# Kernel optimization log

Measured on AMD Instinct MI355X. Metric: run time of the kernel, lower is better.

The kernel has to match this reference:

```python
import jax, jax.numpy as jnp
import numpy as np

NEG_SLOPE = 0.2  # PyG GATConv default negative_slope


def gat_conv(x, src, dst, W, a_src, a_dst, b, n_nodes, concat):
    # x: [N, F_in]; W: [F_in, H*C]; a_src/a_dst: [H, C]; b: [H*C] or [C]
    H, C = a_src.shape
    h = (x @ W).reshape(n_nodes, H, C)                      # [N, H, C]
    al_src = jnp.sum(h * a_src[None], axis=-1)              # [N, H]
    al_dst = jnp.sum(h * a_dst[None], axis=-1)              # [N, H]
    e = jax.nn.leaky_relu(al_src[src] + al_dst[dst], NEG_SLOPE)  # [E, H]
    # segment softmax over incoming edges of each destination node
    m = jax.ops.segment_max(e, dst, num_segments=n_nodes)  # [N, H]
    ex = jnp.exp(e - m[dst])                                # [E, H]
    s = jax.ops.segment_sum(ex, dst, num_segments=n_nodes)  # [N, H]
    alpha = ex / s[dst]                                     # [E, H]
    msg = h[src] * alpha[:, :, None]                        # [E, H, C]
    out = jax.ops.segment_sum(msg, dst, num_segments=n_nodes)  # [N, H, C]
    if concat:
        out = out.reshape(n_nodes, H * C)
    else:
        out = out.mean(axis=1)
    return out + b


def setup_inputs() -> dict:
    key = jax.random.key(0)
    ks = jax.random.split(key, 10)
    N, E = 100000, 800000
    F_in, C1, H, C2 = 128, 32, 8, 16
    x = jax.random.normal(ks[0], (N, F_in), dtype=jnp.float32)
    edge_index = jax.random.randint(ks[1], (2, E), 0, N, dtype=jnp.int64)
    s = 0.05
    return {
        "x": x,
        "edge_index": edge_index,
        "W1": jax.random.normal(ks[2], (F_in, H * C1), dtype=jnp.float32) * s,
        "att_src1": jax.random.normal(ks[3], (H, C1), dtype=jnp.float32) * s,
        "att_dst1": jax.random.normal(ks[4], (H, C1), dtype=jnp.float32) * s,
        "b1": jnp.zeros((H * C1,), dtype=jnp.float32),
        "W2": jax.random.normal(ks[5], (H * C1, H * C2), dtype=jnp.float32) * s,
        "att_src2": jax.random.normal(ks[6], (H, C2), dtype=jnp.float32) * s,
        "att_dst2": jax.random.normal(ks[7], (H, C2), dtype=jnp.float32) * s,
        "b2": jnp.zeros((C2,), dtype=jnp.float32),
    }


def reference(x, edge_index, W1, att_src1, att_dst1, b1, W2, att_src2, att_dst2, b2):
    n = x.shape[0]
    # PyG GATConv default add_self_loops=True (same augmented edge set for both layers)
    loops = jnp.arange(n, dtype=edge_index.dtype)
    src = jnp.concatenate([edge_index[0], loops])
    dst = jnp.concatenate([edge_index[1], loops])
    # dropout_p = 0.0 -> dropout is identity (eval-mode math)
    h = gat_conv(x, src, dst, W1, att_src1, att_dst1, b1, n, concat=True)
    h = jax.nn.elu(h)
    out = gat_conv(h, src, dst, W2, att_src2, att_dst2, b2, n, concat=False)
    return jax.nn.log_softmax(out, axis=-1)
```

## Files before the change

kernel.cpp:

```cpp
#include <hip/hip_runtime.h>
#include <cstdint>
#include <cstddef>


typedef short bf16x8 __attribute__((ext_vector_type(8)));
typedef unsigned short u16x8 __attribute__((ext_vector_type(8)));
typedef float f32x4 __attribute__((ext_vector_type(4)));

__device__ inline unsigned short f2bf(float f) {
  unsigned u = __float_as_uint(f);
  unsigned r = (u + 0x7FFFu + ((u >> 16) & 1u)) >> 16;
  return (unsigned short)r;
}
__device__ inline float bf2f(unsigned short s) {
  return __uint_as_float((unsigned)s << 16);
}

__device__ inline unsigned char fp8enc(float x) {
  unsigned u = __float_as_uint(x);
  unsigned s = u >> 31;
  float ax = fminf(fabsf(x), 448.f);
  unsigned em;
  if (ax >= 0.015625f) {
    unsigned b = __float_as_uint(ax);
    unsigned b2 = b + 0x7FFFFu + ((b >> 20) & 1u);
    em = (b2 >> 20) - 960u;
    if (em > 126u) em = 126u;
  } else {
    em = (unsigned)__float2int_rn(ax * 512.f);
  }
  return (unsigned char)((s << 7) | em);
}
__device__ inline float fp8dec_sw(unsigned b8) {
  unsigned s = b8 >> 7, em = b8 & 0x7Fu;
  float fn = __uint_as_float((s << 31) | ((em + 960u) << 20));
  float fd = (float)em * 0.001953125f;
  fd = s ? -fd : fd;
  return em >= 8u ? fn : fd;
}
__device__ inline void fp8dec4(unsigned w, float* out) {
#if __has_builtin(__builtin_amdgcn_cvt_f32_fp8)
  out[0] = __builtin_amdgcn_cvt_f32_fp8(w, 0);
  out[1] = __builtin_amdgcn_cvt_f32_fp8(w, 1);
  out[2] = __builtin_amdgcn_cvt_f32_fp8(w, 2);
  out[3] = __builtin_amdgcn_cvt_f32_fp8(w, 3);
#else
  out[0] = fp8dec_sw(w & 0xFFu);
  out[1] = fp8dec_sw((w >> 8) & 0xFFu);
  out[2] = fp8dec_sw((w >> 16) & 0xFFu);
  out[3] = fp8dec_sw((w >> 24) & 0xFFu);
#endif
}


__global__ __launch_bounds__(256) void detect_kernel(const int* __restrict__ words,
                                                     int E, int* __restrict__ flag) {
  int t = threadIdx.x;
  int n = E < 1024 ? E : 1024;
  int cnt = 0;
  for (int i = t; i < n; i += 256) cnt += (words[2 * i + 1] != 0) ? 1 : 0;
  for (int m = 1; m < 64; m <<= 1) cnt += __shfl_xor(cnt, m);
  if ((t & 63) == 0 && cnt) atomicAdd(flag, cnt);
}

__global__ __launch_bounds__(256) void extract_kernel(const void* __restrict__ ei,
                                                      int E, int N,
                                                      const int* __restrict__ flag,
                                                      int* __restrict__ src,
                                                      int* __restrict__ dst,
                                                      int* __restrict__ deg) {
  int e = blockIdx.x * 256 + threadIdx.x;
  int ET = E + N;
  if (e >= ET) return;
  int s, d;
  if (e < E) {
    if (flag[0] == 0) {
      const long long* p = (const long long*)ei;
      s = (int)p[e];
      d = (int)p[(size_t)E + e];
    } else {
      const int* p = (const int*)ei;
      s = p[e];
      d = p[E + e];
    }
  } else {
    s = d = e - E;
  }
  src[e] = s;
  dst[e] = d;
  atomicAdd(&deg[d], 1);
}

__global__ __launch_bounds__(256) void scan_a(const int* __restrict__ deg,
                                              int* __restrict__ off,
                                              int* __restrict__ bsum, int N) {
  __shared__ int sh[256];
  int b = blockIdx.x, t = threadIdx.x;
  int base = b * 2048 + t * 8;
  int p[8];
  int run = 0;
#pragma unroll
  for (int j = 0; j < 8; ++j) {
    int v = (base + j < N) ? deg[base + j] : 0;
    run += v;
    p[j] = run;
  }
  sh[t] = run;
  __syncthreads();
  for (int d = 1; d < 256; d <<= 1) {
    int x = (t >= d) ? sh[t - d] : 0;
    __syncthreads();
    if (t >= d) sh[t] += x;
    __syncthreads();
  }
  int excl = sh[t] - run;
#pragma unroll
  for (int j = 0; j < 8; ++j)
    if (base + j < N) off[base + j + 1] = excl + p[j];
  if (t == 255) bsum[b] = sh[255];
}

__global__ void scan_b(int* __restrict__ bsum, int nb) {
  int t = threadIdx.x;
  int orig = (t < nb) ? bsum[t] : 0;
  int v = orig;
  for (int d = 1; d < 64; d <<= 1) {
    int u = __shfl_up(v, d);
    if (t >= d) v += u;
  }
  if (t < nb) bsum[t] = v - orig;
}

__global__ __launch_bounds__(256) void scan_c(int* __restrict__ off,
                                              const int* __restrict__ bsum, int N) {
  int i = blockIdx.x * 256 + threadIdx.x;
  if (i == 0) off[0] = 0;
  if (i >= 1 && i <= N) off[i] += bsum[(i - 1) / 2048];
}

__global__ __launch_bounds__(256) void fill_kernel(const int* __restrict__ src,
                                                   const int* __restrict__ dst,
                                                   const int* __restrict__ off,
                                                   int* __restrict__ deg,
                                                   int* __restrict__ csr, int ET) {
  int e = blockIdx.x * 256 + threadIdx.x;
  if (e >= ET) return;
  int d = dst[e];
  int p = atomicSub(&deg[d], 1) - 1;
  csr[off[d] + p] = src[e];
}

__global__ __launch_bounds__(256) void pack_kernel(const float* __restrict__ W,
                                                   short* __restrict__ Wp,
                                                   int NOUT, int total) {
  int NT = NOUT >> 4;
  for (int idx = blockIdx.x * 256 + threadIdx.x; idx < total;
       idx += gridDim.x * 256) {
    int j = idx & 7;
    int lane = (idx >> 3) & 63;
    int st = idx >> 9;
    int s = st / NT, t = st - s * NT;
    int k = s * 32 + (lane >> 4) * 8 + j;
    int n = t * 16 + (lane & 15);
    Wp[idx] = (short)f2bf(W[(size_t)k * NOUT + n]);
  }
}

template <int K, int NOUT, bool AF32, bool OUT_FP8>
__global__ __launch_bounds__(256) void mfma_gemm(const void* __restrict__ Av,
                                                 const short* __restrict__ Bp,
                                                 short* __restrict__ Cb,
                                                 unsigned char* __restrict__ Cq,
                                                 const float* __restrict__ as,
                                                 const float* __restrict__ ad,
                                                 float* __restrict__ alsO,
                                                 float* __restrict__ aldO, int M) {
  constexpr int KS = K / 32;
  constexpr int NT = NOUT / 16;
  constexpr int RST = NOUT + 8;
  constexpr int QST = NOUT + 16;
  constexpr int C = NOUT / 8;
  __shared__ __align__(16) short lds[64 * RST];
  __shared__ __align__(16) unsigned char ldsq[OUT_FP8 ? 64 * QST : 16];
  const int tid = threadIdx.x;
  const int wave = tid >> 6, lane = tid & 63;
  const int lo = lane & 15, hi = lane >> 4;
  const int rowA = blockIdx.x * 64 + wave * 16 + lo;
  const bool inb = rowA < M;

  f32x4 acc[NT];
#pragma unroll
  for (int t = 0; t < NT; ++t) acc[t] = (f32x4){0.f, 0.f, 0.f, 0.f};

#pragma unroll
  for (int s = 0; s < KS; ++s) {
    bf16x8 af;
    if constexpr (AF32) {
      const float* Ap = (const float*)Av;
      float v[8];
      if (inb) {
        const float4 x0 = *(const float4*)&Ap[(size_t)rowA * K + s * 32 + hi * 8];
        const float4 x1 = *(const float4*)&Ap[(size_t)rowA * K + s * 32 + hi * 8 + 4];
        v[0] = x0.x; v[1] = x0.y; v[2] = x0.z; v[3] = x0.w;
        v[4] = x1.x; v[5] = x1.y; v[6] = x1.z; v[7] = x1.w;
      } else {
#pragma unroll
        for (int j = 0; j < 8; ++j) v[j] = 0.f;
      }
#pragma unroll
      for (int j = 0; j < 8; ++j) af[j] = (short)f2bf(v[j]);
    } else {
      const short* Ab = (const short*)Av;
      if (inb) {
        af = *(const bf16x8*)&Ab[(size_t)rowA * K + s * 32 + hi * 8];
      } else {
#pragma unroll
        for (int j = 0; j < 8; ++j) af[j] = 0;
      }
    }
#pragma unroll
    for (int t = 0; t < NT; ++t) {
      bf16x8 bf = *(const bf16x8*)&Bp[((size_t)(s * NT + t) * 64 + lane) * 8];
      acc[t] = __builtin_amdgcn_mfma_f32_16x16x32_bf16(af, bf, acc[t], 0, 0, 0);
    }
  }

#pragma unroll
  for (int t = 0; t < NT; ++t)
#pragma unroll
    for (int r = 0; r < 4; ++r) {
      int row = wave * 16 + hi * 4 + r;
      lds[row * RST + t * 16 + lo] = (short)f2bf(acc[t][r]);
      if constexpr (OUT_FP8)
        ldsq[row * QST + t * 16 + lo] = fp8enc(acc[t][r]);
    }
  __syncthreads();

  if constexpr (OUT_FP8) {
#pragma unroll
    for (int i = 0; i < (64 * NOUT / 16) / 256; ++i) {
      int v = i * 256 + tid;
      int r = v >> 4;
      int c = v & 15;
      int grow = blockIdx.x * 64 + r;
      if (grow < M)
        *(float4*)&Cq[(size_t)grow * NOUT + c * 16] =
            *(const float4*)&ldsq[r * QST + c * 16];
    }
  } else {
    constexpr int VECS = 64 * NOUT / 8;
#pragma unroll
    for (int i = 0; i < VECS / 256; ++i) {
      int v = i * 256 + tid;
      int r = v / (NOUT / 8);
      int c = v % (NOUT / 8);
      int grow = blockIdx.x * 64 + r;
      if (grow < M)
        *(float4*)&Cb[(size_t)grow * NOUT + c * 8] =
            *(const float4*)&lds[r * RST + c * 8];
    }
  }

  constexpr int SEGS = NOUT / 64;
  if (tid < 64 * SEGS) {
    int r = tid / SEGS, seg = tid % SEGS;
    int grow = blockIdx.x * 64 + r;
    float ps[8], pd[8];
#pragma unroll
    for (int k = 0; k < 8; ++k) { ps[k] = 0.f; pd[k] = 0.f; }
#pragma unroll
    for (int k = 0; k < 8; ++k) {
      int b = seg + SEGS * k;
      u16x8 u = *(const u16x8*)&lds[r * RST + b * 8];
#pragma unroll
      for (int j = 0; j < 8; ++j) {
        float hv = bf2f(u[j]);
        ps[k] = fmaf(hv, as[k * C + seg * 8 + j], ps[k]);
        pd[k] = fmaf(hv, ad[k * C + seg * 8 + j], pd[k]);
      }
    }
#pragma unroll
    for (int d = 1; d < SEGS; d <<= 1)
#pragma unroll
      for (int k = 0; k < 8; ++k) {
        ps[k] += __shfl_xor(ps[k], d);
        pd[k] += __shfl_xor(pd[k], d);
      }
    if (seg == 0 && grow < M) {
      *(float4*)&alsO[(size_t)grow * 8] = make_float4(ps[0], ps[1], ps[2], ps[3]);
      *(float4*)&alsO[(size_t)grow * 8 + 4] = make_float4(ps[4], ps[5], ps[6], ps[7]);
      *(float4*)&aldO[(size_t)grow * 8] = make_float4(pd[0], pd[1], pd[2], pd[3]);
      *(float4*)&aldO[(size_t)grow * 8 + 4] = make_float4(pd[4], pd[5], pd[6], pd[7]);
    }
  }
}

__global__ __launch_bounds__(256) void agg1_kernel(const unsigned char* __restrict__ hq,
                                                   const float* __restrict__ als,
                                                   const float* __restrict__ ald,
                                                   const int* __restrict__ off,
                                                   const int* __restrict__ csr,
                                                   const float* __restrict__ bias,
                                                   short* __restrict__ outb, int N) {
  int wid = blockIdx.x * 4 + (threadIdx.x >> 6);
  if (wid >= N) return;
  int lane = threadIdx.x & 63;
  int rs = off[wid], re = off[wid + 1];
  int es = lane >> 5;
  int gl = lane & 31;
  int head = gl >> 2;
  float aldv = ald[wid * 8 + head];

  float acc[8];
#pragma unroll
  for (int j = 0; j < 8; ++j) acc[j] = 0.f;
  float ws = 0.f;

  int i = rs + es;
  for (; i + 2 < re; i += 4) {
    int s0 = csr[i], s1 = csr[i + 2];
    float e0 = als[s0 * 8 + head] + aldv;
    float e1 = als[s1 * 8 + head] + aldv;
    uint2 u0 = *(const uint2*)&hq[(size_t)s0 * 256 + gl * 8];
    uint2 u1 = *(const uint2*)&hq[(size_t)s1 * 256 + gl * 8];
    e0 = e0 > 0.f ? e0 : 0.2f * e0;
    e1 = e1 > 0.f ? e1 : 0.2f * e1;
    float w0 = __expf(e0), w1 = __expf(e1);
    ws += w0 + w1;
    float d0a[4], d0b[4], d1a[4], d1b[4];
    fp8dec4(u0.x, d0a); fp8dec4(u0.y, d0b);
    fp8dec4(u1.x, d1a); fp8dec4(u1.y, d1b);
#pragma unroll
    for (int j = 0; j < 4; ++j) {
      acc[j] = fmaf(w0, d0a[j], acc[j]);
      acc[j + 4] = fmaf(w0, d0b[j], acc[j + 4]);
      acc[j] = fmaf(w1, d1a[j], acc[j]);
      acc[j + 4] = fmaf(w1, d1b[j], acc[j + 4]);
    }
  }
  if (i < re) {
    int s0 = csr[i];
    float e0 = als[s0 * 8 + head] + aldv;
    uint2 u0 = *(const uint2*)&hq[(size_t)s0 * 256 + gl * 8];
    e0 = e0 > 0.f ? e0 : 0.2f * e0;
    float w0 = __expf(e0);
    ws += w0;
    float d0a[4], d0b[4];
    fp8dec4(u0.x, d0a); fp8dec4(u0.y, d0b);
#pragma unroll
    for (int j = 0; j < 4; ++j) {
      acc[j] = fmaf(w0, d0a[j], acc[j]);
      acc[j + 4] = fmaf(w0, d0b[j], acc[j + 4]);
    }
  }

  ws += __shfl_xor(ws, 32);
#pragma unroll
  for (int j = 0; j < 8; ++j) acc[j] += __shfl_xor(acc[j], 32);
  float inv = 1.f / ws;

  if (lane < 32) {
    u16x8 o;
#pragma unroll
    for (int j = 0; j < 8; ++j) {
      float v = acc[j] * inv + bias[gl * 8 + j];
      o[j] = f2bf(v > 0.f ? v : expm1f(v));
    }
    *(u16x8*)&outb[(size_t)wid * 256 + gl * 8] = o;
  }
}

__global__ __launch_bounds__(256) void agg2_kernel(const short* __restrict__ hb,
                                                   const float* __restrict__ als,
                                                   const float* __restrict__ ald,
                                                   const int* __restrict__ off,
                                                   const int* __restrict__ csr,
                                                   const float* __restrict__ bias,
                                                   float* __restrict__ out, int N) {
  constexpr int LPG = 16;
  constexpr int NS = 4;
  int wid = blockIdx.x * 4 + (threadIdx.x >> 6);
  if (wid >= N) return;
  int lane = threadIdx.x & 63;
  int rs = off[wid], re = off[wid + 1];
  int es = lane / LPG;
  int gl = lane & (LPG - 1);
  int head = gl >> 1;
  float aldv = ald[wid * 8 + head];

  float acc[8];
#pragma unroll
  for (int j = 0; j < 8; ++j) acc[j] = 0.f;
  float ws = 0.f;

  int i = rs + es;
  for (; i + NS < re; i += 2 * NS) {
    int s0 = csr[i], s1 = csr[i + NS];
    float e0 = als[s0 * 8 + head] + aldv;
    float e1 = als[s1 * 8 + head] + aldv;
    u16x8 u0 = *(const u16x8*)&hb[(size_t)s0 * 128 + gl * 8];
    u16x8 u1 = *(const u16x8*)&hb[(size_t)s1 * 128 + gl * 8];
    e0 = e0 > 0.f ? e0 : 0.2f * e0;
    e1 = e1 > 0.f ? e1 : 0.2f * e1;
    float w0 = __expf(e0), w1 = __expf(e1);
    ws += w0 + w1;
#pragma unroll
    for (int j = 0; j < 8; ++j)
      acc[j] = fmaf(w1, bf2f(u1[j]), fmaf(w0, bf2f(u0[j]), acc[j]));
  }
  if (i < re) {
    int s0 = csr[i];
    float e0 = als[s0 * 8 + head] + aldv;
    u16x8 u0 = *(const u16x8*)&hb[(size_t)s0 * 128 + gl * 8];
    e0 = e0 > 0.f ? e0 : 0.2f * e0;
    float w0 = __expf(e0);
    ws += w0;
#pragma unroll
    for (int j = 0; j < 8; ++j) acc[j] = fmaf(w0, bf2f(u0[j]), acc[j]);
  }

#pragma unroll
  for (int d = LPG; d < 64; d <<= 1) {
    ws += __shfl_xor(ws, d);
#pragma unroll
    for (int j = 0; j < 8; ++j) acc[j] += __shfl_xor(acc[j], d);
  }
  float inv = 1.f / ws;

#pragma unroll
  for (int j = 0; j < 8; ++j) acc[j] *= inv;
#pragma unroll
  for (int d = 2; d <= 8; d <<= 1)
#pragma unroll
    for (int j = 0; j < 8; ++j) acc[j] += __shfl_xor(acc[j], d);
  int p = gl & 1;
  float v[8];
#pragma unroll
  for (int j = 0; j < 8; ++j) v[j] = acc[j] * 0.125f + bias[p * 8 + j];
  float m = v[0];
#pragma unroll
  for (int j = 1; j < 8; ++j) m = fmaxf(m, v[j]);
  m = fmaxf(m, __shfl_xor(m, 1));
  float se = 0.f;
#pragma unroll
  for (int j = 0; j < 8; ++j) se += __expf(v[j] - m);
  se += __shfl_xor(se, 1);
  float lse = m + logf(se);
  if (lane < 2) {
    *(float4*)&out[(size_t)wid * 16 + p * 8] =
        make_float4(v[0] - lse, v[1] - lse, v[2] - lse, v[3] - lse);
    *(float4*)&out[(size_t)wid * 16 + p * 8 + 4] =
        make_float4(v[4] - lse, v[5] - lse, v[6] - lse, v[7] - lse);
  }
}


extern "C" void kernel_launch(void* const* d_in, const int* in_sizes, int n_in,
                              void* d_out, int out_size, void* d_ws, size_t ws_size,
                              hipStream_t stream) {
  const float* x = (const float*)d_in[0];
  const void* ei = d_in[1];
  const float* W1 = (const float*)d_in[2];
  const float* as1 = (const float*)d_in[3];
  const float* ad1 = (const float*)d_in[4];
  const float* b1 = (const float*)d_in[5];
  const float* W2 = (const float*)d_in[6];
  const float* as2 = (const float*)d_in[7];
  const float* ad2 = (const float*)d_in[8];
  const float* b2 = (const float*)d_in[9];
  float* out = (float*)d_out;

  const int N = out_size / 16;
  const int E = in_sizes[1] / 2;
  const int ET = E + N;

  char* p = (char*)d_ws;
  auto alloc = [&](size_t bytes) {
    char* r = p;
    p += (bytes + 255) & ~(size_t)255;
    return (void*)r;
  };
  unsigned char* h1q = (unsigned char*)alloc((size_t)N * 256);
  short* hactb = (short*)alloc((size_t)N * 256 * 2);
  short* h2b = (short*)alloc((size_t)N * 128 * 2);
  float* als = (float*)alloc((size_t)N * 8 * 4);
  float* ald = (float*)alloc((size_t)N * 8 * 4);
  int* src32 = (int*)alloc((size_t)ET * 4);
  int* dst32 = (int*)alloc((size_t)ET * 4);
  int* csr = (int*)alloc((size_t)ET * 4);
  int* deg = (int*)alloc((size_t)N * 4);
  int* off = (int*)alloc((size_t)(N + 1) * 4);
  int* bsum = (int*)alloc(256 * 4);
  int* flag = (int*)alloc(256);
  short* W1p = (short*)alloc(128 * 256 * 2);
  short* W2p = (short*)alloc(256 * 128 * 2);

  hipMemsetAsync(deg, 0, (size_t)N * 4, stream);
  hipMemsetAsync(flag, 0, 4, stream);

  detect_kernel<<<1, 256, 0, stream>>>((const int*)ei, E, flag);
  int gridET = (ET + 255) / 256;
  extract_kernel<<<gridET, 256, 0, stream>>>(ei, E, N, flag, src32, dst32, deg);
  int nscan = (N + 2047) / 2048;
  scan_a<<<nscan, 256, 0, stream>>>(deg, off, bsum, N);
  scan_b<<<1, 64, 0, stream>>>(bsum, nscan);
  scan_c<<<(N + 256) / 256, 256, 0, stream>>>(off, bsum, N);
  fill_kernel<<<gridET, 256, 0, stream>>>(src32, dst32, off, deg, csr, ET);

  pack_kernel<<<128, 256, 0, stream>>>(W1, W1p, 256, 128 * 256);
  pack_kernel<<<128, 256, 0, stream>>>(W2, W2p, 128, 256 * 128);

  int gemmGrid = (N + 63) / 64;
  int nodeGrid = (N + 3) / 4;

  mfma_gemm<128, 256, true, true><<<gemmGrid, 256, 0, stream>>>(
      x, W1p, nullptr, h1q, as1, ad1, als, ald, N);
  agg1_kernel<<<nodeGrid, 256, 0, stream>>>(h1q, als, ald, off, csr, b1, hactb, N);
  mfma_gemm<256, 128, false, false><<<gemmGrid, 256, 0, stream>>>(
      hactb, W2p, h2b, nullptr, as2, ad2, als, ald, N);
  agg2_kernel<<<nodeGrid, 256, 0, stream>>>(h2b, als, ald, off, csr, b2, out, N);
}
```

Baseline: 338.5 us.

## Store layer-2 features in fp8 and widen per-lane gathers in aggregation

Layer 2's GEMM now emits fp8 features, reusing the layer-1 fp8 buffer, instead of bf16, so agg2 gathers half the bytes per neighbor. agg1 is restructured so 16 lanes each load 16 bytes per edge and four edge streams run per wave, instead of 32 lanes loading 8 bytes. The two memsets are merged into one by moving the flag allocation next to deg. The aim is to cut the gather traffic that dominates aggregation, at the cost of extra fp8 quantization error in layer 2 and more registers in agg1.

```diff
diff --git a/kernel.cpp b/kernel.cpp
--- a/kernel.cpp
+++ b/kernel.cpp
@@ -237,11 +237,12 @@
   __syncthreads();
 
   if constexpr (OUT_FP8) {
-#pragma unroll
-    for (int i = 0; i < (64 * NOUT / 16) / 256; ++i) {
+    constexpr int CPR = NOUT / 16;
+#pragma unroll
+    for (int i = 0; i < (64 * CPR) / 256; ++i) {
       int v = i * 256 + tid;
-      int r = v >> 4;
-      int c = v & 15;
+      int r = v / CPR;
+      int c = v % CPR;
       int grow = blockIdx.x * 64 + r;
       if (grow < M)
         *(float4*)&Cq[(size_t)grow * NOUT + c * 16] =
@@ -306,85 +307,85 @@
   if (wid >= N) return;
   int lane = threadIdx.x & 63;
   int rs = off[wid], re = off[wid + 1];
-  int es = lane >> 5;
-  int gl = lane & 31;
-  int head = gl >> 2;
+  int es = lane >> 4;
+  int gl = lane & 15;
+  int head = gl >> 1;
   float aldv = ald[wid * 8 + head];
 
-  float acc[8];
-#pragma unroll
-  for (int j = 0; j < 8; ++j) acc[j] = 0.f;
+  float acc[16];
+#pragma unroll
+  for (int j = 0; j < 16; ++j) acc[j] = 0.f;
   float ws = 0.f;
 
   int i = rs + es;
-  for (; i + 2 < re; i += 4) {
-    int s0 = csr[i], s1 = csr[i + 2];
+  for (; i + 4 < re; i += 8) {
+    int s0 = csr[i], s1 = csr[i + 4];
     float e0 = als[s0 * 8 + head] + aldv;
     float e1 = als[s1 * 8 + head] + aldv;
-    uint2 u0 = *(const uint2*)&hq[(size_t)s0 * 256 + gl * 8];
-    uint2 u1 = *(const uint2*)&hq[(size_t)s1 * 256 + gl * 8];
+    uint4 u0 = *(const uint4*)&hq[(size_t)s0 * 256 + gl * 16];
+    uint4 u1 = *(const uint4*)&hq[(size_t)s1 * 256 + gl * 16];
     e0 = e0 > 0.f ? e0 : 0.2f * e0;
     e1 = e1 > 0.f ? e1 : 0.2f * e1;
     float w0 = __expf(e0), w1 = __expf(e1);
     ws += w0 + w1;
-    float d0a[4], d0b[4], d1a[4], d1b[4];
-    fp8dec4(u0.x, d0a); fp8dec4(u0.y, d0b);
-    fp8dec4(u1.x, d1a); fp8dec4(u1.y, d1b);
-#pragma unroll
-    for (int j = 0; j < 4; ++j) {
-      acc[j] = fmaf(w0, d0a[j], acc[j]);
-      acc[j + 4] = fmaf(w0, d0b[j], acc[j + 4]);
-      acc[j] = fmaf(w1, d1a[j], acc[j]);
-      acc[j + 4] = fmaf(w1, d1b[j], acc[j + 4]);
-    }
+    float d0[16], d1[16];
+    fp8dec4(u0.x, d0); fp8dec4(u0.y, d0 + 4);
+    fp8dec4(u0.z, d0 + 8); fp8dec4(u0.w, d0 + 12);
+    fp8dec4(u1.x, d1); fp8dec4(u1.y, d1 + 4);
+    fp8dec4(u1.z, d1 + 8); fp8dec4(u1.w, d1 + 12);
+#pragma unroll
+    for (int j = 0; j < 16; ++j)
+      acc[j] = fmaf(w1, d1[j], fmaf(w0, d0[j], acc[j]));
   }
   if (i < re) {
     int s0 = csr[i];
     float e0 = als[s0 * 8 + head] + aldv;
-    uint2 u0 = *(const uint2*)&hq[(size_t)s0 * 256 + gl * 8];
+    uint4 u0 = *(const uint4*)&hq[(size_t)s0 * 256 + gl * 16];
     e0 = e0 > 0.f ? e0 : 0.2f * e0;
     float w0 = __expf(e0);
     ws += w0;
-    float d0a[4], d0b[4];
-    fp8dec4(u0.x, d0a); fp8dec4(u0.y, d0b);
-#pragma unroll
-    for (int j = 0; j < 4; ++j) {
-      acc[j] = fmaf(w0, d0a[j], acc[j]);
-      acc[j + 4] = fmaf(w0, d0b[j], acc[j + 4]);
-    }
-  }
-
-  ws += __shfl_xor(ws, 32);
-#pragma unroll
-  for (int j = 0; j < 8; ++j) acc[j] += __shfl_xor(acc[j], 32);
+    float d0[16];
+    fp8dec4(u0.x, d0); fp8dec4(u0.y, d0 + 4);
+    fp8dec4(u0.z, d0 + 8); fp8dec4(u0.w, d0 + 12);
+#pragma unroll
+    for (int j = 0; j < 16; ++j) acc[j] = fmaf(w0, d0[j], acc[j]);
+  }
+
+#pragma unroll
+  for (int d = 16; d < 64; d <<= 1) {
+    ws += __shfl_xor(ws, d);
+#pragma unroll
+    for (int j = 0; j < 16; ++j) acc[j] += __shfl_xor(acc[j], d);
+  }
   float inv = 1.f / ws;
 
-  if (lane < 32) {
-    u16x8 o;
+  if (lane < 16) {
+    u16x8 o0, o1;
 #pragma unroll
     for (int j = 0; j < 8; ++j) {
-      float v = acc[j] * inv + bias[gl * 8 + j];
-      o[j] = f2bf(v > 0.f ? v : expm1f(v));
-    }
-    *(u16x8*)&outb[(size_t)wid * 256 + gl * 8] = o;
-  }
-}
-
-__global__ __launch_bounds__(256) void agg2_kernel(const short* __restrict__ hb,
+      float v0 = acc[j] * inv + bias[gl * 16 + j];
+      float v1 = acc[j + 8] * inv + bias[gl * 16 + 8 + j];
+      o0[j] = f2bf(v0 > 0.f ? v0 : expm1f(v0));
+      o1[j] = f2bf(v1 > 0.f ? v1 : expm1f(v1));
+    }
+    *(u16x8*)&outb[(size_t)wid * 256 + gl * 16] = o0;
+    *(u16x8*)&outb[(size_t)wid * 256 + gl * 16 + 8] = o1;
+  }
+}
+
+__global__ __launch_bounds__(256) void agg2_kernel(const unsigned char* __restrict__ hq,
                                                    const float* __restrict__ als,
                                                    const float* __restrict__ ald,
                                                    const int* __restrict__ off,
                                                    const int* __restrict__ csr,
                                                    const float* __restrict__ bias,
                                                    float* __restrict__ out, int N) {
-  constexpr int LPG = 16;
-  constexpr int NS = 4;
   int wid = blockIdx.x * 4 + (threadIdx.x >> 6);
   if (wid >= N) return;
   int lane = threadIdx.x & 63;
   int rs = off[wid], re = off[wid + 1];
-  int es = lane / LPG;
-  int gl = lane & (LPG - 1);
+  int es = lane >> 4;
+  int gl = lane & 15;
   int head = gl >> 1;
   float aldv = ald[wid * 8 + head];
 
@@ -394,33 +395,38 @@
   float ws = 0.f;
 
   int i = rs + es;
-  for (; i + NS < re; i += 2 * NS) {
-    int s0 = csr[i], s1 = csr[i + NS];
+  for (; i + 4 < re; i += 8) {
+    int s0 = csr[i], s1 = csr[i + 4];
     float e0 = als[s0 * 8 + head] + aldv;
     float e1 = als[s1 * 8 + head] + aldv;
-    u16x8 u0 = *(const u16x8*)&hb[(size_t)s0 * 128 + gl * 8];
-    u16x8 u1 = *(const u16x8*)&hb[(size_t)s1 * 128 + gl * 8];
+    uint2 u0 = *(const uint2*)&hq[(size_t)s0 * 128 + gl * 8];
+    uint2 u1 = *(const uint2*)&hq[(size_t)s1 * 128 + gl * 8];
     e0 = e0 > 0.f ? e0 : 0.2f * e0;
     e1 = e1 > 0.f ? e1 : 0.2f * e1;
     float w0 = __expf(e0), w1 = __expf(e1);
     ws += w0 + w1;
+    float d0[8], d1[8];
+    fp8dec4(u0.x, d0); fp8dec4(u0.y, d0 + 4);
+    fp8dec4(u1.x, d1); fp8dec4(u1.y, d1 + 4);
 #pragma unroll
     for (int j = 0; j < 8; ++j)
-      acc[j] = fmaf(w1, bf2f(u1[j]), fmaf(w0, bf2f(u0[j]), acc[j]));
+      acc[j] = fmaf(w1, d1[j], fmaf(w0, d0[j], acc[j]));
   }
   if (i < re) {
     int s0 = csr[i];
     float e0 = als[s0 * 8 + head] + aldv;
-    u16x8 u0 = *(const u16x8*)&hb[(size_t)s0 * 128 + gl * 8];
+    uint2 u0 = *(const uint2*)&hq[(size_t)s0 * 128 + gl * 8];
     e0 = e0 > 0.f ? e0 : 0.2f * e0;
     float w0 = __expf(e0);
     ws += w0;
-#pragma unroll
-    for (int j = 0; j < 8; ++j) acc[j] = fmaf(w0, bf2f(u0[j]), acc[j]);
-  }
-
-#pragma unroll
-  for (int d = LPG; d < 64; d <<= 1) {
+    float d0[8];
+    fp8dec4(u0.x, d0); fp8dec4(u0.y, d0 + 4);
+#pragma unroll
+    for (int j = 0; j < 8; ++j) acc[j] = fmaf(w0, d0[j], acc[j]);
+  }
+
+#pragma unroll
+  for (int d = 16; d < 64; d <<= 1) {
     ws += __shfl_xor(ws, d);
 #pragma unroll
     for (int j = 0; j < 8; ++j) acc[j] += __shfl_xor(acc[j], d);
@@ -482,21 +488,20 @@
   };
   unsigned char* h1q = (unsigned char*)alloc((size_t)N * 256);
   short* hactb = (short*)alloc((size_t)N * 256 * 2);
-  short* h2b = (short*)alloc((size_t)N * 128 * 2);
   float* als = (float*)alloc((size_t)N * 8 * 4);
   float* ald = (float*)alloc((size_t)N * 8 * 4);
   int* src32 = (int*)alloc((size_t)ET * 4);
   int* dst32 = (int*)alloc((size_t)ET * 4);
   int* csr = (int*)alloc((size_t)ET * 4);
   int* deg = (int*)alloc((size_t)N * 4);
+  int* flag = (int*)alloc(256);
   int* off = (int*)alloc((size_t)(N + 1) * 4);
   int* bsum = (int*)alloc(256 * 4);
-  int* flag = (int*)alloc(256);
   short* W1p = (short*)alloc(128 * 256 * 2);
   short* W2p = (short*)alloc(256 * 128 * 2);
-
-  hipMemsetAsync(deg, 0, (size_t)N * 4, stream);
-  hipMemsetAsync(flag, 0, 4, stream);
+  unsigned char* h2q = h1q;
+
+  hipMemsetAsync(deg, 0, (((size_t)N * 4 + 255) & ~(size_t)255) + 4, stream);
 
   detect_kernel<<<1, 256, 0, stream>>>((const int*)ei, E, flag);
   int gridET = (ET + 255) / 256;
@@ -516,7 +521,7 @@
   mfma_gemm<128, 256, true, true><<<gemmGrid, 256, 0, stream>>>(
       x, W1p, nullptr, h1q, as1, ad1, als, ald, N);
   agg1_kernel<<<nodeGrid, 256, 0, stream>>>(h1q, als, ald, off, csr, b1, hactb, N);
-  mfma_gemm<256, 128, false, false><<<gemmGrid, 256, 0, stream>>>(
-      hactb, W2p, h2b, nullptr, as2, ad2, als, ald, N);
-  agg2_kernel<<<nodeGrid, 256, 0, stream>>>(h2b, als, ald, off, csr, b2, out, N);
-}
+  mfma_gemm<256, 128, false, true><<<gemmGrid, 256, 0, stream>>>(
+      hactb, W2p, nullptr, h2q, as2, ad2, als, ald, N);
+  agg2_kernel<<<nodeGrid, 256, 0, stream>>>(h2q, als, ald, off, csr, b2, out, N);
+}
```

Result: slower. 358.9 us (+6.0%).
